# Optimization experiments

Measured on AMD Instinct MI355X. Metric: run time of the kernel, lower is better.

## Reference

```python
import jax, jax.numpy as jnp
import numpy as np

N = 50000       # nodes
E = 500000      # edges (before self-loops)
F_IN = 128      # node feature dim
F_E = 16        # edge feature dim
H = 8           # heads (conv1, conv2)
C1 = 32         # 256 // 8
C2 = 16         # 128 // 8
OUT = 1         # conv3 output channels (1 head, concat=False)
NS = 0.2        # leaky_relu negative slope
EPS = 1e-5      # batchnorm eps


def setup_inputs() -> dict:
    key = jax.random.key(0)
    ks = jax.random.split(key, 32)
    r = lambda k, s: jax.random.normal(k, s, jnp.float32) * 0.1
    inp = {
        'x': jax.random.normal(ks[0], (N, F_IN), jnp.float32),
        'edge_index': jax.random.randint(ks[1], (2, E), 0, N, jnp.int32),
        'edge_attr': jax.random.normal(ks[2], (E, F_E), jnp.float32),
        # conv1 (share_weights=True -> single lin)
        'W1': r(ks[3], (F_IN, H * C1)), 'b1': jnp.zeros((H * C1,), jnp.float32),
        'We1': r(ks[4], (F_E, H * C1)), 'att1': r(ks[5], (H, C1)),
        'bo1': jnp.zeros((H * C1,), jnp.float32),
        'g1': jnp.ones((H * C1,), jnp.float32), 'bt1': jnp.zeros((H * C1,), jnp.float32),
        # conv2 (share_weights=True)
        'W2': r(ks[6], (H * C1, H * C2)), 'b2': jnp.zeros((H * C2,), jnp.float32),
        'We2': r(ks[7], (F_E, H * C2)), 'att2': r(ks[8], (H, C2)),
        'bo2': jnp.zeros((H * C2,), jnp.float32),
        'g2': jnp.ones((H * C2,), jnp.float32), 'bt2': jnp.zeros((H * C2,), jnp.float32),
        # conv3 (share_weights=False -> separate lin_l / lin_r; 1 head, concat=False)
        'W3l': r(ks[9], (H * C2, OUT)), 'b3l': jnp.zeros((OUT,), jnp.float32),
        'W3r': r(ks[10], (H * C2, OUT)), 'b3r': jnp.zeros((OUT,), jnp.float32),
        'We3': r(ks[11], (F_E, OUT)), 'att3': r(ks[12], (1, OUT)),
        'bo3': jnp.zeros((OUT,), jnp.float32),
    }
    return inp


def _gatv2(x, src, dst, eattr, Wl, bl, Wr, br, We, att, bo, heads, ch, concat):
    """One GATv2Conv layer (PyG semantics), edges already include self-loops."""
    n = x.shape[0]
    xl = (x @ Wl + bl).reshape(n, heads, ch)              # source transform
    xr = (x @ Wr + br).reshape(n, heads, ch)              # target transform
    e = (eattr @ We).reshape(-1, heads, ch)               # edge transform (no bias)
    m = xl[src] + xr[dst] + e                             # [Etot, H, C]
    logit = jnp.einsum('ehc,hc->eh', jax.nn.leaky_relu(m, NS), att)
    lmax = jax.ops.segment_max(logit, dst, num_segments=n)
    ex = jnp.exp(logit - lmax[dst])
    denom = jax.ops.segment_sum(ex, dst, num_segments=n)
    alpha = ex / (denom[dst] + 1e-16)                     # segment softmax over dst
    out = jax.ops.segment_sum(alpha[:, :, None] * xl[src], dst, num_segments=n)
    out = out.reshape(n, heads * ch) if concat else out.mean(axis=1)
    return out + bo


def _bn(x, g, b):
    mu = x.mean(axis=0)
    var = ((x - mu) ** 2).mean(axis=0)
    return g * (x - mu) * jax.lax.rsqrt(var + EPS) + b


def reference(x, edge_index, edge_attr, W1, b1, We1, att1, bo1, g1, bt1,
              W2, b2, We2, att2, bo2, g2, bt2,
              W3l, b3l, W3r, b3r, We3, att3, bo3):
    n = x.shape[0]
    # add_self_loops=True with fill_value='mean' for edge_attr (PyG default)
    loop = jnp.arange(n, dtype=edge_index.dtype)
    src = jnp.concatenate([edge_index[0], loop])
    dst = jnp.concatenate([edge_index[1], loop])
    ea = jnp.concatenate([edge_attr,
                          jnp.broadcast_to(edge_attr.mean(axis=0), (n, edge_attr.shape[1]))], axis=0)

    h = _gatv2(x, src, dst, ea, W1, b1, W1, b1, We1, att1, bo1, H, C1, True)
    h = jax.nn.elu(_bn(h, g1, bt1))
    h = _gatv2(h, src, dst, ea, W2, b2, W2, b2, We2, att2, bo2, H, C2, True)
    h = jax.nn.elu(_bn(h, g2, bt2))
    out = _gatv2(h, src, dst, ea, W3l, b3l, W3r, b3r, We3, att3, bo3, 1, OUT, False)
    return out  # [N, 1]
```

## Files before the change

### kernel.cpp

```cpp
#include <hip/hip_runtime.h>

typedef unsigned short u16;
typedef __attribute__((ext_vector_type(4))) float f32x4;
typedef __attribute__((ext_vector_type(2))) float f32x2;
typedef __attribute__((ext_vector_type(8))) short bf16x8;

constexpr int Nn  = 50000;
constexpr int Ee  = 500000;
constexpr int ET  = Nn + Ee;
constexpr int FIN = 128;
constexpr int FE  = 16;
constexpr int Hh  = 8;
constexpr int C1  = 32, HC1 = 256;
constexpr int C2  = 16, HC2 = 128;
constexpr float NS  = 0.2f;
constexpr float EPS = 1e-5f;
constexpr float LOG2E = 1.44269504088896340736f;

__device__ __forceinline__ float b2f(u16 u) { return __uint_as_float(((unsigned)u) << 16); }
__device__ __forceinline__ u16 f2b(float f) {
  unsigned u = __float_as_uint(f);
  u += 0x7FFF + ((u >> 16) & 1);
  return (u16)(u >> 16);
}
__device__ __forceinline__ void stbf2(u16* p, f32x2 v) {
  ushort2 u; u.x = f2b(v.x); u.y = f2b(v.y);
  *reinterpret_cast<ushort2*>(p) = u;
}

template <int RED>
__device__ __forceinline__ float red_sum(float v) {
  v += __int_as_float(__builtin_amdgcn_update_dpp(0, __float_as_int(v), 0xB1, 0xF, 0xF, true));
  v += __int_as_float(__builtin_amdgcn_update_dpp(0, __float_as_int(v), 0x4E, 0xF, 0xF, true));
  v += __int_as_float(__builtin_amdgcn_update_dpp(0, __float_as_int(v), 0x141, 0xF, 0xF, true));
  if constexpr (RED == 16)
    v += __int_as_float(__builtin_amdgcn_update_dpp(0, __float_as_int(v), 0x140, 0xF, 0xF, true));
  return v;
}

__global__ void k_init(int* __restrict__ deg, int* __restrict__ cursor, float* __restrict__ ea_mean,
                       float* __restrict__ bn1s, float* __restrict__ bn1q,
                       float* __restrict__ bn2s, float* __restrict__ bn2q) {
  int t = blockIdx.x * 256 + threadIdx.x;
  int stride = gridDim.x * 256;
  for (int i = t; i < Nn; i += stride) { deg[i] = 0; cursor[i] = 0; }
  if (t < FE) ea_mean[t] = 0.f;
  if (t >= 64 && t < 64 + HC1) { bn1s[t - 64] = 0.f; bn1q[t - 64] = 0.f; }
  if (t >= 384 && t < 384 + HC2) { bn2s[t - 384] = 0.f; bn2q[t - 384] = 0.f; }
}

__global__ void k_deg_mean(const int* __restrict__ ei, const float* __restrict__ ea,
                           int* __restrict__ deg, float* __restrict__ ea_mean) {
  int t = threadIdx.x;
  int e = blockIdx.x * 256 + t;
  if (e < ET) {
    int d = (e < Ee) ? ei[Ee + e] : (e - Ee);
    if ((unsigned)d >= (unsigned)Nn) d = 0;
    atomicAdd(&deg[d], 1);
  }
  __shared__ float s[256];
  int f  = t & 15;
  int r0 = (t >> 4) + blockIdx.x * 16;
  float acc = 0.f;
  for (int r = r0; r < Ee; r += gridDim.x * 16) acc += ea[r * FE + f];
  s[t] = acc;
  __syncthreads();
  if (t < 16) {
    float v = 0.f;
    for (int r = 0; r < 16; r++) v += s[r * 16 + t];
    atomicAdd(&ea_mean[t], v * (1.f / Ee));
  }
}

__global__ __launch_bounds__(1024) void k_scan(const int* __restrict__ deg, int* __restrict__ rowptr) {
  const int T = 1024;
  int t = threadIdx.x;
  const int CH = (Nn + T - 1) / T;
  int base = t * CH;
  int sum = 0;
  for (int i = 0; i < CH; i++) {
    int idx = base + i;
    if (idx < Nn) sum += deg[idx];
  }
  __shared__ int s[T];
  s[t] = sum;
  __syncthreads();
  for (int off = 1; off < T; off <<= 1) {
    int v = (t >= off) ? s[t - off] : 0;
    __syncthreads();
    s[t] += v;
    __syncthreads();
  }
  int run = (t == 0) ? 0 : s[t - 1];
  for (int i = 0; i < CH; i++) {
    int idx = base + i;
    if (idx < Nn) { rowptr[idx] = run; run += deg[idx]; }
  }
  if (t == T - 1) rowptr[Nn] = run;
}

__global__ void k_scatter(const int* __restrict__ ei, const int* __restrict__ rowptr,
                          int* __restrict__ cursor, int2* __restrict__ epack) {
  int e = blockIdx.x * 256 + threadIdx.x;
  if (e >= ET) return;
  if (e < 4) epack[ET + e] = make_int2(0, Ee);
  int s, d;
  if (e < Ee) { s = ei[e]; d = ei[Ee + e]; } else { s = d = e - Ee; }
  if ((unsigned)s >= (unsigned)Nn) s = 0;
  if ((unsigned)d >= (unsigned)Nn) d = 0;
  int pos = rowptr[d] + atomicAdd(&cursor[d], 1);
  epack[pos] = make_int2(s, e);
}

__global__ void k_bn_coef(const float* __restrict__ sum, const float* __restrict__ sq,
                          const float* __restrict__ g, const float* __restrict__ bt,
                          float2* __restrict__ coef, int HC) {
  int ch = threadIdx.x;
  if (ch >= HC) return;
  float mu = sum[ch] * (1.f / Nn);
  float var = sq[ch] * (1.f / Nn) - mu * mu;
  float rs = rsqrtf(var + EPS);
  float sc = g[ch] * rs;
  coef[ch] = make_float2(sc, bt[ch] - sc * mu);
}

template <int HC>
__global__ void k_bn_stats(const u16* __restrict__ x, float* __restrict__ sum, float* __restrict__ sq) {
  long i0 = ((long)blockIdx.x * 256 + threadIdx.x) * 2;
  long stride = (long)gridDim.x * 512;
  float s0 = 0.f, q0 = 0.f, s1 = 0.f, q1 = 0.f;
  for (long e = i0; e < (long)Nn * HC; e += stride) {
    ushort2 u = *reinterpret_cast<const ushort2*>(&x[e]);
    float v0 = b2f(u.x), v1 = b2f(u.y);
    s0 += v0; q0 += v0 * v0; s1 += v1; q1 += v1 * v1;
  }
  int ch = (int)(i0 % HC);
  atomicAdd(&sum[ch], s0); atomicAdd(&sq[ch], q0);
  atomicAdd(&sum[ch + 1], s1); atomicAdd(&sq[ch + 1], q1);
}

template <int KK, int NN, typename AT, bool FUSE>
__global__ __launch_bounds__(256) void k_gemm_mfma(const AT* __restrict__ A, const float* __restrict__ W,
                                                   const float* __restrict__ bias, u16* __restrict__ C,
                                                   const float2* __restrict__ coef, int M) {
  constexpr int WT = KK + 8;
  __shared__ u16 Wt[64 * WT];
  int tid = threadIdx.x;
  int col0 = blockIdx.x * 64;
  int row0 = blockIdx.y * 64;
  for (int idx = tid; idx < KK * 64; idx += 256) {
    int k = idx >> 6, c = idx & 63;
    Wt[c * WT + k] = f2b(W[(size_t)k * NN + col0 + c]);
  }
  __syncthreads();
  int lane = tid & 63;
  int w = tid >> 6;
  int mr = lane & 15, quad = lane >> 4;
  int row = row0 + w * 16 + mr;
  f32x4 acc[4];
#pragma unroll
  for (int t = 0; t < 4; t++) acc[t] = (f32x4){0.f, 0.f, 0.f, 0.f};
  union Frag { bf16x8 v; u16 u[8]; };
  for (int kb = 0; kb < KK; kb += 32) {
    Frag a;
    if (row < M) {
      if constexpr (sizeof(AT) == 4) {
        const float* ap = (const float*)&A[(size_t)row * KK + kb + quad * 8];
        float4 a0 = *reinterpret_cast<const float4*>(ap);
        float4 a1 = *reinterpret_cast<const float4*>(ap + 4);
        a.u[0] = f2b(a0.x); a.u[1] = f2b(a0.y); a.u[2] = f2b(a0.z); a.u[3] = f2b(a0.w);
        a.u[4] = f2b(a1.x); a.u[5] = f2b(a1.y); a.u[6] = f2b(a1.z); a.u[7] = f2b(a1.w);
      } else {
        a.v = *reinterpret_cast<const bf16x8*>(&A[(size_t)row * KK + kb + quad * 8]);
        if constexpr (FUSE) {
          int k0 = kb + quad * 8;
#pragma unroll
          for (int j = 0; j < 8; j++) {
            float2 c2 = coef[k0 + j];
            float y = b2f(a.u[j]) * c2.x + c2.y;
            y = y > 0.f ? y : __expf(y) - 1.f;
            a.u[j] = f2b(y);
          }
        }
      }
    } else {
#pragma unroll
      for (int j = 0; j < 8; j++) a.u[j] = 0;
    }
#pragma unroll
    for (int t = 0; t < 4; t++) {
      const bf16x8* bp = reinterpret_cast<const bf16x8*>(&Wt[(t * 16 + mr) * WT + kb + quad * 8]);
      acc[t] = __builtin_amdgcn_mfma_f32_16x16x32_bf16(a.v, *bp, acc[t], 0, 0, 0);
    }
  }
  int orow = row0 + w * 16 + quad * 4;
#pragma unroll
  for (int t = 0; t < 4; t++) {
    int col = col0 + t * 16 + mr;
    float bs = bias[col];
#pragma unroll
    for (int r = 0; r < 4; r++) {
      int rr = orow + r;
      if (rr < M) C[(size_t)rr * NN + col] = f2b(acc[t][r] + bs);
    }
  }
}

template <int HC, int C, int WPN>
__global__ __launch_bounds__(256) void k_node_attn(
    const int* __restrict__ rowptr, const int2* __restrict__ epack,
    const u16* __restrict__ xl, const float* __restrict__ We, const float* __restrict__ att,
    const float* __restrict__ edge_attr, const float* __restrict__ ea_mean,
    const float* __restrict__ bo, u16* __restrict__ out) {
  __shared__ float sea[4][2][4][16];
  int lane = threadIdx.x & 63;
  int widx = threadIdx.x >> 6;
  int gwid = (blockIdx.x << 2) + widx;
  int nwaves = gridDim.x << 2;
  int w = gwid % WPN;
  int i0 = gwid / WPN;
  int istride = nwaves / WPN;
  int c0 = w * 128 + lane * 2;
  f32x2 w2[FE];
#pragma unroll
  for (int k = 0; k < FE; k++) {
    float2 t = *reinterpret_cast<const float2*>(&We[k * HC + c0]);
    w2[k] = (f32x2){t.x, t.y};
  }
  float at0 = att[c0] * LOG2E, at1 = att[c0 + 1] * LOG2E;
  f32x2 ews2 = {0.f, 0.f};
#pragma unroll
  for (int k = 0; k < FE; k++) ews2 += ea_mean[k] * w2[k];
  float b0 = bo[c0], b1 = bo[c0 + 1];
  constexpr int RED = C / 2;
  constexpr int UN = 4;

  auto stage = [&](const int2* sep, int buf) {
    int y01 = (lane & 4) ? sep[1].y : sep[0].y;
    int y23 = (lane & 4) ? sep[3].y : sep[2].y;
    int eidv = (lane & 8) ? y23 : y01;
    int ec = (eidv < Ee) ? eidv : 0;
    const float* src = edge_attr + (size_t)ec * FE + (lane & 3) * 4;
    if (lane < 16) {
      __builtin_amdgcn_global_load_lds(
          (const __attribute__((address_space(1))) unsigned int*)src,
          (__attribute__((address_space(3))) unsigned int*)&sea[widx][buf][0][0],
          16, 0, 0);
    }
  };
  auto ea_dot_lds = [&](int eid, int buf, int jj) -> f32x2 {
    if (eid < Ee) {
      const float4* ep = reinterpret_cast<const float4*>(&sea[widx][buf][jj][0]);
      f32x2 a = {0.f, 0.f};
#pragma unroll
      for (int k4 = 0; k4 < 4; k4++) {
        float4 u = ep[k4];
        a += u.x * w2[4 * k4 + 0];
        a += u.y * w2[4 * k4 + 1];
        a += u.z * w2[4 * k4 + 2];
        a += u.w * w2[4 * k4 + 3];
      }
      return a;
    }
    return ews2;
  };

  if (i0 >= Nn) return;
  int p0 = rowptr[i0], p1 = rowptr[i0 + 1];
  ushort2 xdr = *reinterpret_cast<const ushort2*>(&xl[(size_t)i0 * HC + c0]);

  for (int i = i0; i < Nn;) {
    int inext = i + istride;
    int np0 = 0, np1 = 0;
    ushort2 nxdr = make_ushort2(0, 0);
    if (inext < Nn) {
      np0 = rowptr[inext];
      np1 = rowptr[inext + 1];
      nxdr = *reinterpret_cast<const ushort2*>(&xl[(size_t)inext * HC + c0]);
    }
    f32x2 xd = (f32x2){b2f(xdr.x), b2f(xdr.y)};
    int nb = (p1 - p0 + UN - 1) >> 2;
    float m = -1e30f, l = 0.f;
    f32x2 acc = {0.f, 0.f};

    int2 se[UN];
#pragma unroll
    for (int j = 0; j < UN; j++) se[j] = epack[p0 + j];
    stage(se, 0);

    int pb = p0;
    for (int b = 0; b < nb; b++) {
      int buf = b & 1;
      asm volatile("s_waitcnt vmcnt(0)" ::: "memory");
      int sA[UN], eA[UN];
#pragma unroll
      for (int j = 0; j < UN; j++) {
        sA[j] = __builtin_amdgcn_readfirstlane(se[j].x);
        eA[j] = __builtin_amdgcn_readfirstlane(se[j].y);
      }
      ushort2 xr[UN];
#pragma unroll
      for (int j = 0; j < UN; j++)
        xr[j] = *reinterpret_cast<const ushort2*>(&xl[(size_t)sA[j] * HC + c0]);
      int pn = pb + UN;
      bool more = pn < p1;
      if (more) {
#pragma unroll
        for (int j = 0; j < UN; j++) se[j] = epack[pn + j];
      }
      f32x2 xs[UN];
      float part[UN];
#pragma unroll
      for (int j = 0; j < UN; j++) {
        f32x2 ew = ea_dot_lds(eA[j], buf, j);
        xs[j] = (f32x2){b2f(xr[j].x), b2f(xr[j].y)};
        f32x2 t = xs[j] + xd + ew;
        f32x2 tn = t * NS;
        f32x2 lk = {fmaxf(t.x, tn.x), fmaxf(t.y, tn.y)};
        float pt = lk.x * at0 + lk.y * at1;
        pt = red_sum<RED>(pt);
        part[j] = (pb + j < p1) ? pt : -1e30f;
      }
      if (more) stage(se, buf ^ 1);
      float mn = m;
#pragma unroll
      for (int j = 0; j < UN; j++) mn = fmaxf(mn, part[j]);
      float sc = __builtin_amdgcn_exp2f(m - mn);
      float a[UN], asum = 0.f;
      f32x2 ax = {0.f, 0.f};
#pragma unroll
      for (int j = 0; j < UN; j++) {
        a[j] = __builtin_amdgcn_exp2f(part[j] - mn);
        asum += a[j];
        ax += a[j] * xs[j];
      }
      l = l * sc + asum;
      acc = acc * sc + ax;
      m = mn;
      pb = pn;
    }
    float inv = 1.f / (l + 1e-16f);
    f32x2 v = {acc.x * inv + b0, acc.y * inv + b1};
    stbf2(&out[(size_t)i * HC + c0], v);
    i = inext; p0 = np0; p1 = np1; xdr = nxdr;
  }
}

__global__ __launch_bounds__(256) void k_gemv3(const u16* __restrict__ h2,
                                               const float2* __restrict__ coef,
                                               const float* __restrict__ W3l, const float* __restrict__ b3l,
                                               const float* __restrict__ W3r, const float* __restrict__ b3r,
                                               float* __restrict__ xl3, float* __restrict__ xr3) {
  int lane = threadIdx.x & 63;
  int i = (blockIdx.x << 2) + (threadIdx.x >> 6);
  if (i >= Nn) return;
  float2 ca = coef[lane], cb = coef[64 + lane];
  float a = b2f(h2[(long)i * HC2 + lane]) * ca.x + ca.y;
  a = a > 0.f ? a : __expf(a) - 1.f;
  float b = b2f(h2[(long)i * HC2 + 64 + lane]) * cb.x + cb.y;
  b = b > 0.f ? b : __expf(b) - 1.f;
  float pl = a * W3l[lane] + b * W3l[64 + lane];
  float pr = a * W3r[lane] + b * W3r[64 + lane];
  for (int o = 1; o < 64; o <<= 1) { pl += __shfl_xor(pl, o); pr += __shfl_xor(pr, o); }
  if (lane == 0) { xl3[i] = pl + b3l[0]; xr3[i] = pr + b3r[0]; }
}

__global__ __launch_bounds__(256) void k_final3(
    const int* __restrict__ rowptr, const int2* __restrict__ epack,
    const float* __restrict__ xl3, const float* __restrict__ xr3,
    const float* __restrict__ We3, const float* __restrict__ att3,
    const float* __restrict__ edge_attr, const float* __restrict__ ea_mean,
    const float* __restrict__ bo3, float* __restrict__ out) {
  int t = threadIdx.x;
  int lane16 = t & 15;
  int i = blockIdx.x * 16 + (t >> 4);
  if (i >= Nn) return;
  float we[FE];
#pragma unroll
  for (int k4 = 0; k4 < 4; k4++) {
    float4 u = reinterpret_cast<const float4*>(We3)[k4];
    we[4 * k4] = u.x; we[4 * k4 + 1] = u.y; we[4 * k4 + 2] = u.z; we[4 * k4 + 3] = u.w;
  }
  float at = att3[0];
  float ews = 0.f;
#pragma unroll
  for (int k = 0; k < FE; k++) ews += ea_mean[k] * we[k];
  float xd = xr3[i];
  int p0 = rowptr[i], p1 = rowptr[i + 1];
  float m = -1e30f, l = 0.f, o = 0.f;
  for (int p = p0 + lane16; p < p1; p += 16) {
    int2 se = epack[p];
    int s = se.x, eid = se.y;
    float ew;
    if (eid < Ee) {
      const float4* ep = reinterpret_cast<const float4*>(&edge_attr[(size_t)eid * FE]);
      ew = 0.f;
#pragma unroll
      for (int k4 = 0; k4 < 4; k4++) {
        float4 u = ep[k4];
        ew += u.x * we[4 * k4] + u.y * we[4 * k4 + 1] + u.z * we[4 * k4 + 2] + u.w * we[4 * k4 + 3];
      }
    } else ew = ews;
    float xsv = xl3[s];
    float tt = xsv + xd + ew;
    float v = tt > 0.f ? tt : NS * tt;
    float logit = v * at;
    float mn = fmaxf(m, logit);
    float sc = __expf(m - mn);
    float a = __expf(logit - mn);
    l = l * sc + a;
    o = o * sc + a * xsv;
    m = mn;
  }
  float M = m;
#pragma unroll
  for (int off = 1; off < 16; off <<= 1) M = fmaxf(M, __shfl_xor(M, off));
  float adj = __expf(m - M);
  float lw = l * adj, ow = o * adj;
#pragma unroll
  for (int off = 1; off < 16; off <<= 1) { lw += __shfl_xor(lw, off); ow += __shfl_xor(ow, off); }
  if (lane16 == 0) out[i] = ow / (lw + 1e-16f) + bo3[0];
}

extern "C" void kernel_launch(void* const* d_in, const int* in_sizes, int n_in,
                              void* d_out, int out_size, void* d_ws, size_t ws_size,
                              hipStream_t stream) {
  const float* x    = (const float*)d_in[0];
  const int*   ei   = (const int*)d_in[1];
  const float* ea   = (const float*)d_in[2];
  const float* W1   = (const float*)d_in[3];
  const float* b1   = (const float*)d_in[4];
  const float* We1  = (const float*)d_in[5];
  const float* att1 = (const float*)d_in[6];
  const float* bo1  = (const float*)d_in[7];
  const float* g1   = (const float*)d_in[8];
  const float* bt1  = (const float*)d_in[9];
  const float* W2   = (const float*)d_in[10];
  const float* b2   = (const float*)d_in[11];
  const float* We2  = (const float*)d_in[12];
  const float* att2 = (const float*)d_in[13];
  const float* bo2  = (const float*)d_in[14];
  const float* g2   = (const float*)d_in[15];
  const float* bt2  = (const float*)d_in[16];
  const float* W3l  = (const float*)d_in[17];
  const float* b3l  = (const float*)d_in[18];
  const float* W3r  = (const float*)d_in[19];
  const float* b3r  = (const float*)d_in[20];
  const float* We3  = (const float*)d_in[21];
  const float* att3 = (const float*)d_in[22];
  const float* bo3  = (const float*)d_in[23];
  float* out = (float*)d_out;

  char* ws = (char*)d_ws;
  size_t off = 0;
  auto alloc = [&](size_t bytes) -> void* {
    void* p = ws + off;
    off = (off + bytes + 255) & ~(size_t)255;
    return p;
  };
  int*    deg     = (int*)alloc((size_t)Nn * 4);
  int*    rowptr  = (int*)alloc((size_t)(Nn + 1) * 4);
  int*    cursor  = (int*)alloc((size_t)Nn * 4);
  int2*   epack   = (int2*)alloc((size_t)(ET + 4) * 8);
  float*  ea_mean = (float*)alloc((size_t)FE * 4);
  float*  bn1s    = (float*)alloc(256 * 4);
  float*  bn1q    = (float*)alloc(256 * 4);
  float*  bn2s    = (float*)alloc(128 * 4);
  float*  bn2q    = (float*)alloc(128 * 4);
  float2* bncoef  = (float2*)alloc(256 * 8);
  float*  xl3     = (float*)alloc((size_t)Nn * 4);
  float*  xr3     = (float*)alloc((size_t)Nn * 4);
  u16*    xlA     = (u16*)alloc((size_t)Nn * 256 * 2);
  u16*    hB      = (u16*)alloc((size_t)Nn * 256 * 2);

  k_init<<<512, 256, 0, stream>>>(deg, cursor, ea_mean, bn1s, bn1q, bn2s, bn2q);
  k_deg_mean<<<(ET + 255) / 256, 256, 0, stream>>>(ei, ea, deg, ea_mean);
  k_scan<<<1, 1024, 0, stream>>>(deg, rowptr);
  k_scatter<<<(ET + 255) / 256, 256, 0, stream>>>(ei, rowptr, cursor, epack);

  k_gemm_mfma<FIN, HC1, float, false><<<dim3(HC1 / 64, (Nn + 63) / 64), 256, 0, stream>>>(
      x, W1, b1, xlA, nullptr, Nn);
  k_node_attn<HC1, C1, 2><<<2048, 256, 0, stream>>>(rowptr, epack, xlA, We1, att1,
                                                    ea, ea_mean, bo1, hB);
  k_bn_stats<HC1><<<256, 256, 0, stream>>>(hB, bn1s, bn1q);
  k_bn_coef<<<1, 256, 0, stream>>>(bn1s, bn1q, g1, bt1, bncoef, HC1);

  k_gemm_mfma<HC1, HC2, u16, true><<<dim3(HC2 / 64, (Nn + 63) / 64), 256, 0, stream>>>(
      hB, W2, b2, xlA, bncoef, Nn);
  k_node_attn<HC2, C2, 1><<<2048, 256, 0, stream>>>(rowptr, epack, xlA, We2, att2,
                                                    ea, ea_mean, bo2, hB);
  k_bn_stats<HC2><<<256, 256, 0, stream>>>(hB, bn2s, bn2q);
  k_bn_coef<<<1, 256, 0, stream>>>(bn2s, bn2q, g2, bt2, bncoef, HC2);

  k_gemv3<<<(Nn + 3) / 4, 256, 0, stream>>>(hB, bncoef, W3l, b3l, W3r, b3r, xl3, xr3);
  k_final3<<<(Nn + 15) / 16, 256, 0, stream>>>(rowptr, epack, xl3, xr3, We3, att3,
                                               ea, ea_mean, bo3, out);
}
```

Measured before the change: 728.1 us.

## Fuse batchnorm statistics into attention kernel and use packed FP32 math

Removes the separate k_bn_stats passes by accumulating per-channel sum and sum-of-squares of the bf16-rounded outputs inside k_node_attn, then doing one atomicAdd per channel per wave at the end. This avoids re-reading the 25.6MB and 12.8MB hidden tensors and saves two launches. It also rewrites the edge-attribute dot product and the leaky-relu pre-activation with inline v_pk_fma/v_pk_add/v_pk_mul asm to halve the VALU instruction count. The cost is extra atomics (2048*4 waves, each adding to a few channels) contending on a small set of addresses, plus inline asm that the compiler cannot schedule around.

```diff
diff --git a/kernel.cpp b/kernel.cpp
--- a/kernel.cpp
+++ b/kernel.cpp
@@ -28,6 +28,27 @@
   *reinterpret_cast<ushort2*>(p) = u;
 }
 
+__device__ __forceinline__ f32x2 pk_fma_lo(f32x2 s, f32x2 w, f32x2 acc) {
+  asm("v_pk_fma_f32 %0, %1, %2, %0 op_sel:[0,0,0] op_sel_hi:[0,1,1]"
+      : "+v"(acc) : "v"(s), "v"(w));
+  return acc;
+}
+__device__ __forceinline__ f32x2 pk_fma_hi(f32x2 s, f32x2 w, f32x2 acc) {
+  asm("v_pk_fma_f32 %0, %1, %2, %0 op_sel:[1,0,0] op_sel_hi:[1,1,1]"
+      : "+v"(acc) : "v"(s), "v"(w));
+  return acc;
+}
+__device__ __forceinline__ f32x2 pk_add(f32x2 a, f32x2 b) {
+  f32x2 d;
+  asm("v_pk_add_f32 %0, %1, %2" : "=v"(d) : "v"(a), "v"(b));
+  return d;
+}
+__device__ __forceinline__ f32x2 pk_mul(f32x2 a, f32x2 b) {
+  f32x2 d;
+  asm("v_pk_mul_f32 %0, %1, %2" : "=v"(d) : "v"(a), "v"(b));
+  return d;
+}
+
 template <int RED>
 __device__ __forceinline__ float red_sum(float v) {
   v += __int_as_float(__builtin_amdgcn_update_dpp(0, __float_as_int(v), 0xB1, 0xF, 0xF, true));
@@ -122,21 +143,6 @@
   float rs = rsqrtf(var + EPS);
   float sc = g[ch] * rs;
   coef[ch] = make_float2(sc, bt[ch] - sc * mu);
-}
-
-template <int HC>
-__global__ void k_bn_stats(const u16* __restrict__ x, float* __restrict__ sum, float* __restrict__ sq) {
-  long i0 = ((long)blockIdx.x * 256 + threadIdx.x) * 2;
-  long stride = (long)gridDim.x * 512;
-  float s0 = 0.f, q0 = 0.f, s1 = 0.f, q1 = 0.f;
-  for (long e = i0; e < (long)Nn * HC; e += stride) {
-    ushort2 u = *reinterpret_cast<const ushort2*>(&x[e]);
-    float v0 = b2f(u.x), v1 = b2f(u.y);
-    s0 += v0; q0 += v0 * v0; s1 += v1; q1 += v1 * v1;
-  }
-  int ch = (int)(i0 % HC);
-  atomicAdd(&sum[ch], s0); atomicAdd(&sq[ch], q0);
-  atomicAdd(&sum[ch + 1], s1); atomicAdd(&sq[ch + 1], q1);
 }
 
 template <int KK, int NN, typename AT, bool FUSE>
@@ -211,7 +217,8 @@
     const int* __restrict__ rowptr, const int2* __restrict__ epack,
     const u16* __restrict__ xl, const float* __restrict__ We, const float* __restrict__ att,
     const float* __restrict__ edge_attr, const float* __restrict__ ea_mean,
-    const float* __restrict__ bo, u16* __restrict__ out) {
+    const float* __restrict__ bo, u16* __restrict__ out,
+    float* __restrict__ bnsum, float* __restrict__ bnsq) {
   __shared__ float sea[4][2][4][16];
   int lane = threadIdx.x & 63;
   int widx = threadIdx.x >> 6;
@@ -232,6 +239,7 @@
 #pragma unroll
   for (int k = 0; k < FE; k++) ews2 += ea_mean[k] * w2[k];
   float b0 = bo[c0], b1 = bo[c0 + 1];
+  const f32x2 ns2 = {NS, NS};
   constexpr int RED = C / 2;
   constexpr int UN = 4;
 
@@ -255,10 +263,12 @@
 #pragma unroll
       for (int k4 = 0; k4 < 4; k4++) {
         float4 u = ep[k4];
-        a += u.x * w2[4 * k4 + 0];
-        a += u.y * w2[4 * k4 + 1];
-        a += u.z * w2[4 * k4 + 2];
-        a += u.w * w2[4 * k4 + 3];
+        f32x2 pA = {u.x, u.y};
+        f32x2 pB = {u.z, u.w};
+        a = pk_fma_lo(pA, w2[4 * k4 + 0], a);
+        a = pk_fma_hi(pA, w2[4 * k4 + 1], a);
+        a = pk_fma_lo(pB, w2[4 * k4 + 2], a);
+        a = pk_fma_hi(pB, w2[4 * k4 + 3], a);
       }
       return a;
     }
@@ -268,6 +278,7 @@
   if (i0 >= Nn) return;
   int p0 = rowptr[i0], p1 = rowptr[i0 + 1];
   ushort2 xdr = *reinterpret_cast<const ushort2*>(&xl[(size_t)i0 * HC + c0]);
+  float bs0 = 0.f, bq0 = 0.f, bs1 = 0.f, bq1 = 0.f;
 
   for (int i = i0; i < Nn;) {
     int inext = i + istride;
@@ -314,17 +325,15 @@
       for (int j = 0; j < UN; j++) {
         f32x2 ew = ea_dot_lds(eA[j], buf, j);
         xs[j] = (f32x2){b2f(xr[j].x), b2f(xr[j].y)};
-        f32x2 t = xs[j] + xd + ew;
-        f32x2 tn = t * NS;
-        f32x2 lk = {fmaxf(t.x, tn.x), fmaxf(t.y, tn.y)};
-        float pt = lk.x * at0 + lk.y * at1;
+        f32x2 t = pk_add(pk_add(xs[j], xd), ew);
+        f32x2 tn = pk_mul(t, ns2);
+        float lk0 = fmaxf(t.x, tn.x), lk1 = fmaxf(t.y, tn.y);
+        float pt = lk0 * at0 + lk1 * at1;
         pt = red_sum<RED>(pt);
         part[j] = (pb + j < p1) ? pt : -1e30f;
       }
       if (more) stage(se, buf ^ 1);
-      float mn = m;
-#pragma unroll
-      for (int j = 0; j < UN; j++) mn = fmaxf(mn, part[j]);
+      float mn = fmaxf(fmaxf(m, part[0]), fmaxf(fmaxf(part[1], part[2]), part[3]));
       float sc = __builtin_amdgcn_exp2f(m - mn);
       float a[UN], asum = 0.f;
       f32x2 ax = {0.f, 0.f};
@@ -341,9 +350,15 @@
     }
     float inv = 1.f / (l + 1e-16f);
     f32x2 v = {acc.x * inv + b0, acc.y * inv + b1};
-    stbf2(&out[(size_t)i * HC + c0], v);
+    u16 r0 = f2b(v.x), r1 = f2b(v.y);
+    ushort2 ru; ru.x = r0; ru.y = r1;
+    *reinterpret_cast<ushort2*>(&out[(size_t)i * HC + c0]) = ru;
+    float v0 = b2f(r0), v1 = b2f(r1);
+    bs0 += v0; bq0 += v0 * v0; bs1 += v1; bq1 += v1 * v1;
     i = inext; p0 = np0; p1 = np1; xdr = nxdr;
   }
+  atomicAdd(&bnsum[c0], bs0);     atomicAdd(&bnsq[c0], bq0);
+  atomicAdd(&bnsum[c0 + 1], bs1); atomicAdd(&bnsq[c0 + 1], bq1);
 }
 
 __global__ __launch_bounds__(256) void k_gemv3(const u16* __restrict__ h2,
@@ -481,15 +496,13 @@
   k_gemm_mfma<FIN, HC1, float, false><<<dim3(HC1 / 64, (Nn + 63) / 64), 256, 0, stream>>>(
       x, W1, b1, xlA, nullptr, Nn);
   k_node_attn<HC1, C1, 2><<<2048, 256, 0, stream>>>(rowptr, epack, xlA, We1, att1,
-                                                    ea, ea_mean, bo1, hB);
-  k_bn_stats<HC1><<<256, 256, 0, stream>>>(hB, bn1s, bn1q);
+                                                    ea, ea_mean, bo1, hB, bn1s, bn1q);
   k_bn_coef<<<1, 256, 0, stream>>>(bn1s, bn1q, g1, bt1, bncoef, HC1);
 
   k_gemm_mfma<HC1, HC2, u16, true><<<dim3(HC2 / 64, (Nn + 63) / 64), 256, 0, stream>>>(
       hB, W2, b2, xlA, bncoef, Nn);
   k_node_attn<HC2, C2, 1><<<2048, 256, 0, stream>>>(rowptr, epack, xlA, We2, att2,
-                                                    ea, ea_mean, bo2, hB);
-  k_bn_stats<HC2><<<256, 256, 0, stream>>>(hB, bn2s, bn2q);
+                                                    ea, ea_mean, bo2, hB, bn2s, bn2q);
   k_bn_coef<<<1, 256, 0, stream>>>(bn2s, bn2q, g2, bt2, bncoef, HC2);
 
   k_gemv3<<<(Nn + 3) / 4, 256, 0, stream>>>(hB, bncoef, W3l, b3l, W3r, b3r, xl3, xr3);
```

Result: slower. 1.069 ms (+46.8%).
